# Performance work log

Hardware: AMD Instinct MI355X
Metric: run time of the kernel (lower is better)

The kernel has to match this reference:

```python
import jax, jax.numpy as jnp
import numpy as np


def setup_inputs() -> dict:
    key = jax.random.key(0)
    ks = jax.random.split(key, 6)
    B, H, F, X, T = 8, 32, 8, 128, 256
    z0 = jax.random.normal(ks[0], (B, H, X), jnp.float32)
    xi = jax.random.normal(ks[1], (B, F, X, T), jnp.float32)
    A = jax.random.normal(ks[2], (H, H), jnp.float32) * 0.1
    Gw = jax.random.normal(ks[3], (H, F, H), jnp.float32) * 0.1
    Wr = jax.random.normal(ks[4], (X, H, H, H), jnp.float32) * 1e-4
    Wi = jax.random.normal(ks[5], (X, H, H, H), jnp.float32) * 1e-4
    return {"z0": z0, "xi": xi, "A": A, "Gw": Gw, "Wr": Wr, "Wi": Wi}


def reference(z0, xi, A, Gw, Wr, Wi):
    # z0: (B, H, X); xi: (B, F, X, T)
    B, Hc, X = z0.shape
    T = xi.shape[-1]

    # Initial guess u(t) = z0 for all t (reconstruction of the fixed-point seed).
    u = jnp.broadcast_to(z0[..., None], (B, Hc, X, T))

    # Linear SPDE right-hand side: Fu = A u, Gu = Gw u.
    Fu = jnp.einsum('ih,bhxt->bixt', A, u)
    Gu = jnp.einsum('ifh,bhxt->bifxt', Gw, u)          # (B, H, F, X, T)
    Guxi = jnpum = None
    Guxi = jnp.einsum('bifxt,bfxt->bixt', Gu, xi)
    Hu = Fu + Guxi                                      # (B, H, X, T)

    # Spatial FFT (axis 2) + fftshift, as in the torch module.
    H_ft = jnp.fft.fftshift(jnp.fft.fft(Hu, axis=2), axes=2)    # complex64
    z0_ft = jnp.fft.fftshift(jnp.fft.fft(z0, axis=2), axes=2)   # (B, H, X)

    # Per-Fourier-mode complex-linear CDE vector field weights.
    W = (Wr + 1j * Wi).astype(jnp.complex64)            # (X, H, H, H)

    # Control path X(t): (B, X, T, H); Euler increments at the knots.
    Hp = jnp.transpose(H_ft, (0, 2, 3, 1))
    dX = Hp[:, :, 1:, :] - Hp[:, :, :-1, :]             # (B, X, T-1, H)
    z_init = jnp.transpose(z0_ft, (0, 2, 1))            # (B, X, H)

    def step(z, dx):
        # f(z)[b, x, i, c] = sum_j W[x, i, c, j] z[b, x, j]
        fz = jnp.einsum('xicj,bxj->bxic', W, z)
        z_new = z + jnp.einsum('bxic,bxc->bxi', fz, dx)  # dz = f(z) . dX
        return z_new, z_new

    _, zs = jax.lax.scan(step, z_init, jnp.moveaxis(dX, 2, 0))
    zs = jnp.concatenate([z_init[None], zs], axis=0)    # (T, B, X, H)
    z_all = jnp.transpose(zs, (1, 3, 2, 0))             # (B, H, X, T)

    u_new = jnp.fft.ifft(jnp.fft.ifftshift(z_all, axes=2), axis=2)
    return u_new.real
```

## Files before the change

### kernel.cpp

```cpp
#include <hip/hip_runtime.h>
#include <math.h>

#define Bc 8
#define Hc 32
#define Fc 8
#define Xc 128
#define Tc 256

typedef __bf16 bf16x8 __attribute__((ext_vector_type(8)));
typedef float f32x4 __attribute__((ext_vector_type(4)));

__device__ __forceinline__ int bitrev7(int x) { return (int)(__brev((unsigned)x) >> 25); }

__device__ __forceinline__ unsigned pack_bf16(float a, float b) {
    unsigned ua = __float_as_uint(a);
    unsigned ub = __float_as_uint(b);
    ua = (ua + 0x7FFFu + ((ua >> 16) & 1u)) >> 16;
    ub = (ub + 0x7FFFu + ((ub >> 16) & 1u)) & 0xFFFF0000u;
    return (ua & 0xFFFFu) | ub;
}
__device__ __forceinline__ float bf16_val(float a) {
    unsigned ua = __float_as_uint(a);
    ua = (ua + 0x7FFFu + ((ua >> 16) & 1u)) & 0xFFFF0000u;
    return __uint_as_float(ua);
}

__device__ __forceinline__ void fft32x128(float2* buf, float sign) {
    __shared__ float2 tw[128];
    int tid = threadIdx.x;
    if (tid >= 1 && tid < 128) {
        int h = 1 << (31 - __builtin_clz((unsigned)tid));
        int pos = tid - h;
        float sn, cs;
        __sincosf(3.14159265358979f * (float)pos / (float)h, &sn, &cs);
        tw[tid] = make_float2(cs, sn);
    }
    for (int half = 1; half < 128; half <<= 1) {
        __syncthreads();
        for (int g = threadIdx.x; g < 32 * 64; g += 256) {
            int row = g >> 6, j = g & 63;
            int pos = j & (half - 1);
            int i0 = ((j & ~(half - 1)) << 1) + pos;
            float2* p = buf + row * 128;
            float2 a = p[i0];
            float2 bb = p[i0 + half];
            float2 twv = tw[half + pos];
            float cs = twv.x, sn = sign * twv.y;
            float2 bw = make_float2(cs * bb.x - sn * bb.y, cs * bb.y + sn * bb.x);
            p[i0] = make_float2(a.x + bw.x, a.y + bw.y);
            p[i0 + half] = make_float2(a.x - bw.x, a.y - bw.y);
        }
    }
    __syncthreads();
}

__global__ void k_xit(const float* __restrict__ xi, float* __restrict__ xiT) {
    __shared__ float tile[32][33];
    int bid = blockIdx.x;
    int bf = bid >> 3, tt = bid & 7;
    int t0 = tt * 32;
    int tid = threadIdx.x;
    for (int xt = 0; xt < 4; ++xt) {
        int x0 = xt * 32;
        __syncthreads();
        for (int idx = tid; idx < 1024; idx += 256) {
            int xr = idx >> 5, tc = idx & 31;
            tile[xr][tc] = xi[((size_t)bf * Xc + x0 + xr) * Tc + t0 + tc];
        }
        __syncthreads();
        for (int idx = tid; idx < 1024; idx += 256) {
            int tr = idx >> 5, xc = idx & 31;
            xiT[((size_t)bf * Tc + t0 + tr) * Xc + x0 + xc] = tile[xc][tr];
        }
    }
}

__global__ void k_pre(const float* __restrict__ z0, const float* __restrict__ A,
                      const float* __restrict__ Gw, float* __restrict__ Fz,
                      float* __restrict__ Gz, float2* __restrict__ Z0ft) {
    __shared__ float z0l[Hc * Xc];
    __shared__ float2 cbuf[Hc * Xc];
    int b = blockIdx.x;
    int tid = threadIdx.x;
    for (int idx = tid; idx < Hc * Xc; idx += 256) z0l[idx] = z0[b * Hc * Xc + idx];
    __syncthreads();
    for (int idx = tid; idx < Hc * Xc; idx += 256) {
        int i = idx >> 7, x = idx & 127;
        float s = 0.f;
        for (int h = 0; h < Hc; ++h) s += A[i * Hc + h] * z0l[h * 128 + x];
        Fz[b * Hc * Xc + idx] = s;
    }
    for (int idx = tid; idx < Hc * Fc * Xc; idx += 256) {
        int i = idx >> 10, f = (idx >> 7) & 7, x = idx & 127;
        float s = 0.f;
        for (int h = 0; h < Hc; ++h) s += Gw[(i * Fc + f) * Hc + h] * z0l[h * 128 + x];
        Gz[b * Hc * Fc * Xc + idx] = s;
    }
    for (int idx = tid; idx < Hc * Xc; idx += 256) {
        int h = idx >> 7, x = idx & 127;
        cbuf[h * 128 + bitrev7(x)] = make_float2(z0l[h * 128 + x], 0.f);
    }
    fft32x128(cbuf, -1.f);
    for (int idx = tid; idx < Xc * Hc; idx += 256) {
        int xs = idx >> 5, h = idx & 31;
        Z0ft[(b * Xc + xs) * Hc + h] = cbuf[h * 128 + ((xs + 64) & 127)];
    }
}

__global__ void k_spec(const float* __restrict__ xiT, const float* __restrict__ Fz,
                       const float* __restrict__ Gz, float2* __restrict__ Hft) {
    __shared__ float xil[Fc * Xc];
    __shared__ float2 cbuf[Hc * Xc];
    int bid = blockIdx.x;
    int b = bid >> 8, t = bid & 255;
    int tid = threadIdx.x;
    for (int idx = tid; idx < Fc * Xc; idx += 256) {
        int f = idx >> 7, x = idx & 127;
        xil[idx] = xiT[((size_t)(b * Fc + f) * Tc + t) * Xc + x];
    }
    __syncthreads();
    for (int idx = tid; idx < Hc * Xc; idx += 256) {
        int i = idx >> 7, x = idx & 127;
        float hu = Fz[b * Hc * Xc + idx];
        const float* gzp = Gz + (b * Hc + i) * (Fc * Xc) + x;
#pragma unroll
        for (int f = 0; f < Fc; ++f) hu += gzp[f * 128] * xil[f * 128 + x];
        cbuf[i * 128 + bitrev7(x)] = make_float2(hu, 0.f);
    }
    fft32x128(cbuf, -1.f);
    for (int idx = tid; idx < Xc * Hc; idx += 256) {
        int xs = idx >> 5, i = idx & 31;
        Hft[((long)(b * Xc + xs) * Tc + t) * Hc + i] = cbuf[i * 128 + ((xs + 64) & 127)];
    }
}

#define ML_DW 16448
#define B_DW  1152
#define SCAN_LDS 150016

__device__ __forceinline__ void build_B(unsigned* Bb, int w, int tt, int c,
                                        float2 hp, float2 hn, float sc) {
    float dre = (hn.x - hp.x) * sc;
    float dim = (hn.y - hp.y) * sc;
    float hre = bf16_val(dre), hmim = bf16_val(-dim), him = bf16_val(dim);
    int n0 = w * 4 + tt * 2;
    Bb[n0 * 36 + c] = pack_bf16(hre, hmim);
    Bb[(n0 + 1) * 36 + c] = pack_bf16(him, hre);
    Bb[576 + n0 * 36 + c] = pack_bf16(dre - hre, (-dim) - hmim);
    Bb[576 + (n0 + 1) * 36 + c] = pack_bf16(dim - him, dre - hre);
}

__global__ __launch_bounds__(768, 3) void k_scan(const float* __restrict__ Wr,
                                                 const float* __restrict__ Wi,
                                                 const float2* __restrict__ Hft,
                                                 const float2* __restrict__ Z0ft,
                                                 float2* __restrict__ Zall) {
    extern __shared__ unsigned char smem[];
    float* Mlf = (float*)smem;
    unsigned* Aw = (unsigned*)smem;
    unsigned* Bd = (unsigned*)(smem + 131584);
    float* zlf = (float*)(smem + 140800);
    float2* zstc = (float2*)(smem + 141824);

    int tid = threadIdx.x;
    int x = blockIdx.x >> 1, g = blockIdx.x & 1;
    int lane = tid & 63, wid = tid >> 6;
    int isProd = (wid < 8);
    int p = wid;
    int w = isProd ? (wid & 3) : (wid - 8);
    int b = g * 4 + w;

    const float* wrp = Wr + (size_t)x * 32768;
    const float* wip = Wi + (size_t)x * 32768;
    for (int idx = tid; idx < 32768; idx += 768) {
        int j = idx & 31, cc = (idx >> 5) & 31, ii = idx >> 10;
        int r = ii * 32 + j;
        int pd = r * 32 + (((cc >> 2) ^ (r & 7)) << 2) + (cc & 3);
        Aw[pd] = pack_bf16(wrp[(ii * 32 + cc) * 32 + j], wip[(ii * 32 + cc) * 32 + j]);
    }
    __syncthreads();

    size_t bx = (size_t)(b * Xc + x);
    const float2* Hrow = Hft + bx * (Tc * Hc);
    float2* Zrow = Zall + bx * (Hc * Tc);
    int jq = lane >> 5, il = lane & 31;

    uint4 af[8][2];
    float2 Hp2 = make_float2(0.f, 0.f), Hn2 = make_float2(0.f, 0.f);
    float2 zr = make_float2(0.f, 0.f);

    if (isProd) {
        int n16 = lane & 15, q = lane >> 4;
        int rbase = p * 128 + n16;
#pragma unroll
        for (int mt = 0; mt < 8; ++mt) {
            int r = rbase + mt * 16;
#pragma unroll
            for (int kf = 0; kf < 2; ++kf) {
                int cg = (kf * 4 + q) ^ (r & 7);
                af[mt][kf] = *(const uint4*)(Aw + r * 32 + cg * 4);
            }
        }
        if (p < 4) {
            float2 ha = Hrow[jq * 32 + il];
            float2 hb = Hrow[(1 + jq) * 32 + il];
            build_B(Bd, w, jq, il, ha, hb, 1.f);
            Hp2 = Hrow[(2 + jq) * 32 + il];
            Hn2 = Hrow[(3 + jq) * 32 + il];
        }
    } else {
        zr = Z0ft[bx * Hc + il];
        if (jq == 0) {
            ((float2*)(zlf + w * 64))[il] = zr;
            zstc[w * 256 + il] = zr;
        }
    }
    __syncthreads();

#pragma unroll 1
    for (int k = 0; k <= 128; ++k) {
        if (isProd) {
            if (k < 128) {
                int bk = k & 1;
                {
                    int n = lane & 15, q = lane >> 4;
                    const unsigned* Bb = Bd + bk * B_DW;
                    bf16x8 bh0 = __builtin_bit_cast(bf16x8, *(const uint4*)(Bb + n * 36 + q * 4));
                    bf16x8 bh1 = __builtin_bit_cast(bf16x8, *(const uint4*)(Bb + n * 36 + 16 + q * 4));
                    bf16x8 bl0 = __builtin_bit_cast(bf16x8, *(const uint4*)(Bb + 576 + n * 36 + q * 4));
                    bf16x8 bl1 = __builtin_bit_cast(bf16x8, *(const uint4*)(Bb + 576 + n * 36 + 16 + q * 4));
                    float* Mb = Mlf + bk * ML_DW;
#pragma unroll
                    for (int mt = 0; mt < 8; ++mt) {
                        f32x4 acc = {0.f, 0.f, 0.f, 0.f};
                        acc = __builtin_amdgcn_mfma_f32_16x16x32_bf16(
                            __builtin_bit_cast(bf16x8, af[mt][0]), bh0, acc, 0, 0, 0);
                        acc = __builtin_amdgcn_mfma_f32_16x16x32_bf16(
                            __builtin_bit_cast(bf16x8, af[mt][1]), bh1, acc, 0, 0, 0);
                        acc = __builtin_amdgcn_mfma_f32_16x16x32_bf16(
                            __builtin_bit_cast(bf16x8, af[mt][0]), bl0, acc, 0, 0, 0);
                        acc = __builtin_amdgcn_mfma_f32_16x16x32_bf16(
                            __builtin_bit_cast(bf16x8, af[mt][1]), bl1, acc, 0, 0, 0);
                        int i = p * 4 + (mt >> 1);
                        int jgp = (((mt & 1) * 4) + q) ^ (i & 7);
                        *(f32x4*)(Mb + n * 1028 + i * 32 + jgp * 4) = acc;
                    }
                }
                if (p < 4) {
                    if (k < 127) {
                        float sc = (2 * (k + 1) + 1 + jq <= 255) ? 1.f : 0.f;
                        build_B(Bd + ((k + 1) & 1) * B_DW, w, jq, il, Hp2, Hn2, sc);
                    }
                    if (k < 126) {
                        int kc = k + 2;
                        Hp2 = Hrow[(2 * kc + jq) * 32 + il];
                        int t2 = 2 * kc + 1 + jq;
                        if (t2 > 255) t2 = 255;
                        Hn2 = Hrow[t2 * 32 + il];
                    }
                }
            }
        } else if (k > 0) {
            int kc = k - 1;
            int bk = kc & 1;
#pragma unroll
            for (int s = 0; s < 2; ++s) {
                int t = 2 * kc + 1 + s;
                if (t > 255) break;
                const float* base = Mlf + bk * ML_DW + (w * 4 + s * 2) * 1028 + il * 32;
                float4 mr[4], mi[4];
#pragma unroll
                for (int gg = 0; gg < 4; ++gg) {
                    int jg = (((jq * 4 + gg) ^ (il & 7)) << 2);
                    mr[gg] = *(const float4*)(base + jg);
                    mi[gg] = *(const float4*)(base + 1028 + jg);
                }
                const float4* zf4 = (const float4*)(zlf + w * 64);
                float yR = 0.f, yI = 0.f;
#pragma unroll
                for (int gg = 0; gg < 4; ++gg) {
                    float4 za = zf4[jq * 8 + gg * 2];
                    float4 zb = zf4[jq * 8 + gg * 2 + 1];
                    yR += mr[gg].x * za.x - mi[gg].x * za.y + mr[gg].y * za.z - mi[gg].y * za.w
                        + mr[gg].z * zb.x - mi[gg].z * zb.y + mr[gg].w * zb.z - mi[gg].w * zb.w;
                    yI += mr[gg].x * za.y + mi[gg].x * za.x + mr[gg].y * za.w + mi[gg].y * za.z
                        + mr[gg].z * zb.y + mi[gg].z * zb.x + mr[gg].w * zb.w + mi[gg].w * zb.z;
                }
                yR += __shfl_xor(yR, 32);
                yI += __shfl_xor(yI, 32);
                zr.x += yR;
                zr.y += yI;
                if (jq == 0) {
                    ((float2*)(zlf + w * 64))[il] = zr;
                    zstc[w * 256 + (t & 7) * 32 + il] = zr;
                }
                if ((t & 7) == 7) {
                    int t0 = t - 7;
                    int i2 = lane >> 1, tb = (lane & 1) * 4;
                    float2 v0 = zstc[w * 256 + (tb + 0) * 32 + i2];
                    float2 v1 = zstc[w * 256 + (tb + 1) * 32 + i2];
                    float2 v2 = zstc[w * 256 + (tb + 2) * 32 + i2];
                    float2 v3 = zstc[w * 256 + (tb + 3) * 32 + i2];
                    *(float4*)(Zrow + i2 * Tc + t0 + tb) = make_float4(v0.x, v0.y, v1.x, v1.y);
                    *(float4*)(Zrow + i2 * Tc + t0 + tb + 2) = make_float4(v2.x, v2.y, v3.x, v3.y);
                }
            }
        }
        __syncthreads();
    }
}

__global__ void k_post(const float2* __restrict__ Zall, float* __restrict__ out) {
    __shared__ float2 cbuf[32 * 128];
    int bid = blockIdx.x;
    int b = bid >> 8, i = (bid >> 3) & 31, tq = bid & 7;
    int t0 = tq * 32;
    int tid = threadIdx.x;
    for (int idx = tid; idx < 128 * 32; idx += 256) {
        int k = idx >> 5, tc = idx & 31;
        int xg = (k + 64) & 127;
        cbuf[tc * 128 + bitrev7(k)] =
            Zall[((long)(b * Xc + xg) * Hc + i) * Tc + t0 + tc];
    }
    fft32x128(cbuf, +1.f);
    const float inv = 1.0f / 128.0f;
    for (int idx = tid; idx < 128 * 32; idx += 256) {
        int xs = idx >> 5, tc = idx & 31;
        out[((long)(b * Hc + i) * Xc + xs) * Tc + t0 + tc] = cbuf[tc * 128 + xs].x * inv;
    }
}

extern "C" void kernel_launch(void* const* d_in, const int* in_sizes, int n_in,
                              void* d_out, int out_size, void* d_ws, size_t ws_size,
                              hipStream_t stream) {
    const float* z0 = (const float*)d_in[0];
    const float* xi = (const float*)d_in[1];
    const float* A = (const float*)d_in[2];
    const float* Gw = (const float*)d_in[3];
    const float* Wr = (const float*)d_in[4];
    const float* Wi = (const float*)d_in[5];
    float* out = (float*)d_out;
    char* ws = (char*)d_ws;

    float2* Hft = (float2*)(ws);
    float2* Zall = (float2*)(ws + 67108864);
    float2* Z0ft = (float2*)(ws + 134217728);
    float* Fz = (float*)(ws + 134479872);
    float* Gz = (float*)(ws + 134610944);
    float* xiT = (float*)(ws + 67108864);

    (void)hipFuncSetAttribute((const void*)k_scan,
                              hipFuncAttributeMaxDynamicSharedMemorySize, SCAN_LDS);

    k_xit<<<Bc * Fc * 8, 256, 0, stream>>>(xi, xiT);
    k_pre<<<Bc, 256, 0, stream>>>(z0, A, Gw, Fz, Gz, Z0ft);
    k_spec<<<Bc * Tc, 256, 0, stream>>>(xiT, Fz, Gz, Hft);
    k_scan<<<Xc * 2, 768, SCAN_LDS, stream>>>(Wr, Wi, Hft, Z0ft, Zall);
    k_post<<<Bc * Hc * 8, 256, 0, stream>>>(Zall, out);
}
```

Baseline: 463.4 us.

## Move B-operand construction to consumer warps in scan; double threads for FFT kernels

```diff
diff --git a/kernel.cpp b/kernel.cpp
--- a/kernel.cpp
+++ b/kernel.cpp
@@ -25,6 +25,7 @@
     return __uint_as_float(ua);
 }
 
+template <int NTHR>
 __device__ __forceinline__ void fft32x128(float2* buf, float sign) {
     __shared__ float2 tw[128];
     int tid = threadIdx.x;
@@ -37,7 +38,7 @@
     }
     for (int half = 1; half < 128; half <<= 1) {
         __syncthreads();
-        for (int g = threadIdx.x; g < 32 * 64; g += 256) {
+        for (int g = threadIdx.x; g < 32 * 64; g += NTHR) {
             int row = g >> 6, j = g & 63;
             int pos = j & (half - 1);
             int i0 = ((j & ~(half - 1)) << 1) + pos;
@@ -100,7 +101,7 @@
         int h = idx >> 7, x = idx & 127;
         cbuf[h * 128 + bitrev7(x)] = make_float2(z0l[h * 128 + x], 0.f);
     }
-    fft32x128(cbuf, -1.f);
+    fft32x128<256>(cbuf, -1.f);
     for (int idx = tid; idx < Xc * Hc; idx += 256) {
         int xs = idx >> 5, h = idx & 31;
         Z0ft[(b * Xc + xs) * Hc + h] = cbuf[h * 128 + ((xs + 64) & 127)];
@@ -114,12 +115,12 @@
     int bid = blockIdx.x;
     int b = bid >> 8, t = bid & 255;
     int tid = threadIdx.x;
-    for (int idx = tid; idx < Fc * Xc; idx += 256) {
+    for (int idx = tid; idx < Fc * Xc; idx += 512) {
         int f = idx >> 7, x = idx & 127;
         xil[idx] = xiT[((size_t)(b * Fc + f) * Tc + t) * Xc + x];
     }
     __syncthreads();
-    for (int idx = tid; idx < Hc * Xc; idx += 256) {
+    for (int idx = tid; idx < Hc * Xc; idx += 512) {
         int i = idx >> 7, x = idx & 127;
         float hu = Fz[b * Hc * Xc + idx];
         const float* gzp = Gz + (b * Hc + i) * (Fc * Xc) + x;
@@ -127,8 +128,8 @@
         for (int f = 0; f < Fc; ++f) hu += gzp[f * 128] * xil[f * 128 + x];
         cbuf[i * 128 + bitrev7(x)] = make_float2(hu, 0.f);
     }
-    fft32x128(cbuf, -1.f);
-    for (int idx = tid; idx < Xc * Hc; idx += 256) {
+    fft32x128<512>(cbuf, -1.f);
+    for (int idx = tid; idx < Xc * Hc; idx += 512) {
         int xs = idx >> 5, i = idx & 31;
         Hft[((long)(b * Xc + xs) * Tc + t) * Hc + i] = cbuf[i * 128 + ((xs + 64) & 127)];
     }
@@ -201,19 +202,17 @@
                 af[mt][kf] = *(const uint4*)(Aw + r * 32 + cg * 4);
             }
         }
-        if (p < 4) {
-            float2 ha = Hrow[jq * 32 + il];
-            float2 hb = Hrow[(1 + jq) * 32 + il];
-            build_B(Bd, w, jq, il, ha, hb, 1.f);
-            Hp2 = Hrow[(2 + jq) * 32 + il];
-            Hn2 = Hrow[(3 + jq) * 32 + il];
-        }
     } else {
         zr = Z0ft[bx * Hc + il];
         if (jq == 0) {
             ((float2*)(zlf + w * 64))[il] = zr;
             zstc[w * 256 + il] = zr;
         }
+        float2 ha = Hrow[jq * 32 + il];
+        float2 hb = Hrow[(1 + jq) * 32 + il];
+        build_B(Bd, w, jq, il, ha, hb, 1.f);
+        Hp2 = Hrow[(2 + jq) * 32 + il];
+        Hn2 = Hrow[(3 + jq) * 32 + il];
     }
     __syncthreads();
 
@@ -222,88 +221,89 @@
         if (isProd) {
             if (k < 128) {
                 int bk = k & 1;
-                {
-                    int n = lane & 15, q = lane >> 4;
-                    const unsigned* Bb = Bd + bk * B_DW;
-                    bf16x8 bh0 = __builtin_bit_cast(bf16x8, *(const uint4*)(Bb + n * 36 + q * 4));
-                    bf16x8 bh1 = __builtin_bit_cast(bf16x8, *(const uint4*)(Bb + n * 36 + 16 + q * 4));
-                    bf16x8 bl0 = __builtin_bit_cast(bf16x8, *(const uint4*)(Bb + 576 + n * 36 + q * 4));
-                    bf16x8 bl1 = __builtin_bit_cast(bf16x8, *(const uint4*)(Bb + 576 + n * 36 + 16 + q * 4));
-                    float* Mb = Mlf + bk * ML_DW;
-#pragma unroll
-                    for (int mt = 0; mt < 8; ++mt) {
-                        f32x4 acc = {0.f, 0.f, 0.f, 0.f};
-                        acc = __builtin_amdgcn_mfma_f32_16x16x32_bf16(
-                            __builtin_bit_cast(bf16x8, af[mt][0]), bh0, acc, 0, 0, 0);
-                        acc = __builtin_amdgcn_mfma_f32_16x16x32_bf16(
-                            __builtin_bit_cast(bf16x8, af[mt][1]), bh1, acc, 0, 0, 0);
-                        acc = __builtin_amdgcn_mfma_f32_16x16x32_bf16(
-                            __builtin_bit_cast(bf16x8, af[mt][0]), bl0, acc, 0, 0, 0);
-                        acc = __builtin_amdgcn_mfma_f32_16x16x32_bf16(
-                            __builtin_bit_cast(bf16x8, af[mt][1]), bl1, acc, 0, 0, 0);
-                        int i = p * 4 + (mt >> 1);
-                        int jgp = (((mt & 1) * 4) + q) ^ (i & 7);
-                        *(f32x4*)(Mb + n * 1028 + i * 32 + jgp * 4) = acc;
+                int n = lane & 15, q = lane >> 4;
+                const unsigned* Bb = Bd + bk * B_DW;
+                bf16x8 bh0 = __builtin_bit_cast(bf16x8, *(const uint4*)(Bb + n * 36 + q * 4));
+                bf16x8 bh1 = __builtin_bit_cast(bf16x8, *(const uint4*)(Bb + n * 36 + 16 + q * 4));
+                bf16x8 bl0 = __builtin_bit_cast(bf16x8, *(const uint4*)(Bb + 576 + n * 36 + q * 4));
+                bf16x8 bl1 = __builtin_bit_cast(bf16x8, *(const uint4*)(Bb + 576 + n * 36 + 16 + q * 4));
+                float* Mb = Mlf + bk * ML_DW;
+#pragma unroll
+                for (int mt = 0; mt < 8; ++mt) {
+                    f32x4 acc = {0.f, 0.f, 0.f, 0.f};
+                    acc = __builtin_amdgcn_mfma_f32_16x16x32_bf16(
+                        __builtin_bit_cast(bf16x8, af[mt][0]), bh0, acc, 0, 0, 0);
+                    acc = __builtin_amdgcn_mfma_f32_16x16x32_bf16(
+                        __builtin_bit_cast(bf16x8, af[mt][1]), bh1, acc, 0, 0, 0);
+                    acc = __builtin_amdgcn_mfma_f32_16x16x32_bf16(
+                        __builtin_bit_cast(bf16x8, af[mt][0]), bl0, acc, 0, 0, 0);
+                    acc = __builtin_amdgcn_mfma_f32_16x16x32_bf16(
+                        __builtin_bit_cast(bf16x8, af[mt][1]), bl1, acc, 0, 0, 0);
+                    int i = p * 4 + (mt >> 1);
+                    int jgp = (((mt & 1) * 4) + q) ^ (i & 7);
+                    *(f32x4*)(Mb + n * 1028 + i * 32 + jgp * 4) = acc;
+                }
+            }
+        } else {
+            float2 HpN = Hp2, HnN = Hn2;
+            if (k + 2 <= 127) {
+                int kc2 = k + 2;
+                HpN = Hrow[(2 * kc2 + jq) * 32 + il];
+                int t2 = 2 * kc2 + 1 + jq;
+                if (t2 > 255) t2 = 255;
+                HnN = Hrow[t2 * 32 + il];
+            }
+            if (k > 0) {
+                int kc = k - 1;
+                int bk = kc & 1;
+#pragma unroll
+                for (int s = 0; s < 2; ++s) {
+                    int t = 2 * kc + 1 + s;
+                    if (t > 255) break;
+                    const float* base = Mlf + bk * ML_DW + (w * 4 + s * 2) * 1028 + il * 32;
+                    float4 mr[4], mi[4];
+#pragma unroll
+                    for (int gg = 0; gg < 4; ++gg) {
+                        int jg = (((jq * 4 + gg) ^ (il & 7)) << 2);
+                        mr[gg] = *(const float4*)(base + jg);
+                        mi[gg] = *(const float4*)(base + 1028 + jg);
+                    }
+                    const float4* zf4 = (const float4*)(zlf + w * 64);
+                    float yR = 0.f, yI = 0.f;
+#pragma unroll
+                    for (int gg = 0; gg < 4; ++gg) {
+                        float4 za = zf4[jq * 8 + gg * 2];
+                        float4 zb = zf4[jq * 8 + gg * 2 + 1];
+                        yR += mr[gg].x * za.x - mi[gg].x * za.y + mr[gg].y * za.z - mi[gg].y * za.w
+                            + mr[gg].z * zb.x - mi[gg].z * zb.y + mr[gg].w * zb.z - mi[gg].w * zb.w;
+                        yI += mr[gg].x * za.y + mi[gg].x * za.x + mr[gg].y * za.w + mi[gg].y * za.z
+                            + mr[gg].z * zb.y + mi[gg].z * zb.x + mr[gg].w * zb.w + mi[gg].w * zb.z;
+                    }
+                    yR += __shfl_xor(yR, 32);
+                    yI += __shfl_xor(yI, 32);
+                    zr.x += yR;
+                    zr.y += yI;
+                    if (jq == 0) {
+                        ((float2*)(zlf + w * 64))[il] = zr;
+                        zstc[w * 256 + (t & 7) * 32 + il] = zr;
+                    }
+                    if ((t & 7) == 7) {
+                        int t0 = t - 7;
+                        int i2 = lane >> 1, tb = (lane & 1) * 4;
+                        float2 v0 = zstc[w * 256 + (tb + 0) * 32 + i2];
+                        float2 v1 = zstc[w * 256 + (tb + 1) * 32 + i2];
+                        float2 v2 = zstc[w * 256 + (tb + 2) * 32 + i2];
+                        float2 v3 = zstc[w * 256 + (tb + 3) * 32 + i2];
+                        *(float4*)(Zrow + i2 * Tc + t0 + tb) = make_float4(v0.x, v0.y, v1.x, v1.y);
+                        *(float4*)(Zrow + i2 * Tc + t0 + tb + 2) = make_float4(v2.x, v2.y, v3.x, v3.y);
                     }
                 }
-                if (p < 4) {
-                    if (k < 127) {
-                        float sc = (2 * (k + 1) + 1 + jq <= 255) ? 1.f : 0.f;
-                        build_B(Bd + ((k + 1) & 1) * B_DW, w, jq, il, Hp2, Hn2, sc);
-                    }
-                    if (k < 126) {
-                        int kc = k + 2;
-                        Hp2 = Hrow[(2 * kc + jq) * 32 + il];
-                        int t2 = 2 * kc + 1 + jq;
-                        if (t2 > 255) t2 = 255;
-                        Hn2 = Hrow[t2 * 32 + il];
-                    }
-                }
-            }
-        } else if (k > 0) {
-            int kc = k - 1;
-            int bk = kc & 1;
-#pragma unroll
-            for (int s = 0; s < 2; ++s) {
-                int t = 2 * kc + 1 + s;
-                if (t > 255) break;
-                const float* base = Mlf + bk * ML_DW + (w * 4 + s * 2) * 1028 + il * 32;
-                float4 mr[4], mi[4];
-#pragma unroll
-                for (int gg = 0; gg < 4; ++gg) {
-                    int jg = (((jq * 4 + gg) ^ (il & 7)) << 2);
-                    mr[gg] = *(const float4*)(base + jg);
-                    mi[gg] = *(const float4*)(base + 1028 + jg);
-                }
-                const float4* zf4 = (const float4*)(zlf + w * 64);
-                float yR = 0.f, yI = 0.f;
-#pragma unroll
-                for (int gg = 0; gg < 4; ++gg) {
-                    float4 za = zf4[jq * 8 + gg * 2];
-                    float4 zb = zf4[jq * 8 + gg * 2 + 1];
-                    yR += mr[gg].x * za.x - mi[gg].x * za.y + mr[gg].y * za.z - mi[gg].y * za.w
-                        + mr[gg].z * zb.x - mi[gg].z * zb.y + mr[gg].w * zb.z - mi[gg].w * zb.w;
-                    yI += mr[gg].x * za.y + mi[gg].x * za.x + mr[gg].y * za.w + mi[gg].y * za.z
-                        + mr[gg].z * zb.y + mi[gg].z * zb.x + mr[gg].w * zb.w + mi[gg].w * zb.z;
-                }
-                yR += __shfl_xor(yR, 32);
-                yI += __shfl_xor(yI, 32);
-                zr.x += yR;
-                zr.y += yI;
-                if (jq == 0) {
-                    ((float2*)(zlf + w * 64))[il] = zr;
-                    zstc[w * 256 + (t & 7) * 32 + il] = zr;
-                }
-                if ((t & 7) == 7) {
-                    int t0 = t - 7;
-                    int i2 = lane >> 1, tb = (lane & 1) * 4;
-                    float2 v0 = zstc[w * 256 + (tb + 0) * 32 + i2];
-                    float2 v1 = zstc[w * 256 + (tb + 1) * 32 + i2];
-                    float2 v2 = zstc[w * 256 + (tb + 2) * 32 + i2];
-                    float2 v3 = zstc[w * 256 + (tb + 3) * 32 + i2];
-                    *(float4*)(Zrow + i2 * Tc + t0 + tb) = make_float4(v0.x, v0.y, v1.x, v1.y);
-                    *(float4*)(Zrow + i2 * Tc + t0 + tb + 2) = make_float4(v2.x, v2.y, v3.x, v3.y);
-                }
+            }
+            if (k < 127) {
+                float sc = (2 * (k + 1) + 1 + jq <= 255) ? 1.f : 0.f;
+                build_B(Bd + ((k + 1) & 1) * B_DW, w, jq, il, Hp2, Hn2, sc);
+                Hp2 = HpN;
+                Hn2 = HnN;
             }
         }
         __syncthreads();
@@ -316,15 +316,15 @@
     int b = bid >> 8, i = (bid >> 3) & 31, tq = bid & 7;
     int t0 = tq * 32;
     int tid = threadIdx.x;
-    for (int idx = tid; idx < 128 * 32; idx += 256) {
+    for (int idx = tid; idx < 128 * 32; idx += 512) {
         int k = idx >> 5, tc = idx & 31;
         int xg = (k + 64) & 127;
         cbuf[tc * 128 + bitrev7(k)] =
             Zall[((long)(b * Xc + xg) * Hc + i) * Tc + t0 + tc];
     }
-    fft32x128(cbuf, +1.f);
+    fft32x128<512>(cbuf, +1.f);
     const float inv = 1.0f / 128.0f;
-    for (int idx = tid; idx < 128 * 32; idx += 256) {
+    for (int idx = tid; idx < 128 * 32; idx += 512) {
         int xs = idx >> 5, tc = idx & 31;
         out[((long)(b * Hc + i) * Xc + xs) * Tc + t0 + tc] = cbuf[tc * 128 + xs].x * inv;
     }
@@ -354,7 +354,7 @@
 
     k_xit<<<Bc * Fc * 8, 256, 0, stream>>>(xi, xiT);
     k_pre<<<Bc, 256, 0, stream>>>(z0, A, Gw, Fz, Gz, Z0ft);
-    k_spec<<<Bc * Tc, 256, 0, stream>>>(xiT, Fz, Gz, Hft);
+    k_spec<<<Bc * Tc, 512, 0, stream>>>(xiT, Fz, Gz, Hft);
     k_scan<<<Xc * 2, 768, SCAN_LDS, stream>>>(Wr, Wi, Hft, Z0ft, Zall);
-    k_post<<<Bc * Hc * 8, 256, 0, stream>>>(Zall, out);
-}
+    k_post<<<Bc * Hc * 8, 512, 0, stream>>>(Zall, out);
+}
```

New measurement: 471.2 us. No clear change (+1.7%).
